# Kernel optimization log

Measured on AMD Instinct MI355X. Metric: run time of the kernel, lower is better.

The kernel has to match this reference:

```python
import jax, jax.numpy as jnp
import numpy as np
import math

L, R, B, S, D = 103, 512, 2, 512, 768


def setup_inputs() -> dict:
    key = jax.random.key(0)
    ks = jax.random.split(key, 16)
    n = lambda k, sh, s=1.0: jax.random.normal(k, sh, jnp.float32) * s
    W = 0.02  # weight init scale keeps softmax logits well-conditioned
    return {
        "output": n(ks[0], (B, S, D)),              # BERT sequence output (backbone treated as feature extractor)
        "attention_mask": jnp.ones((B, S), jnp.int32),
        "laws": n(ks[1], (L, R, D)),                # precomputed law representations (laws_rep.pkl)
        "Wq": n(ks[2], (D, D), W), "bq": jnp.zeros((D,), jnp.float32),
        "Wk": n(ks[3], (D, D), W), "bk": jnp.zeros((D,), jnp.float32),
        "Wv": n(ks[4], (D, D), W), "bv": jnp.zeros((D,), jnp.float32),
        "w_law_d": n(ks[5], (D,), W), "b_law_d": jnp.zeros((1,), jnp.float32),
        "w_law1": n(ks[6], (R,), W), "b_law1": jnp.zeros((1,), jnp.float32),
        "w_accu_d": n(ks[7], (D,), W), "b_accu_d": jnp.zeros((1,), jnp.float32),
        "w_accu1": n(ks[8], (R,), W), "b_accu1": jnp.zeros((1,), jnp.float32),
        "W_accu2": n(ks[9], (119, L), W), "b_accu2": jnp.zeros((119,), jnp.float32),
        "w_term_d": n(ks[10], (D,), W), "b_term_d": jnp.zeros((1,), jnp.float32),
        "w_term1": n(ks[11], (R,), W), "b_term1": jnp.zeros((1,), jnp.float32),
        "W_term2": n(ks[12], (11, L), W), "b_term2": jnp.zeros((11,), jnp.float32),
    }


def _forward(output, mask_f, laws, Wq, bq, Wk, bk, Wv, bv,
             w_law_d, b_law_d, w_law1, b_law1,
             w_accu_d, b_accu_d, w_accu1, b_accu1, W_accu2, b_accu2,
             w_term_d, b_term_d, w_term1, b_term1, W_term2, b_term2):
    laws_q = laws @ Wq + bq          # [L,R,D]
    facts_k = output @ Wk + bk       # [B,S,D]
    facts_v = output @ Wv + bv       # [B,S,D]
    # relevance: [L,B,R,S]
    scores = jnp.einsum('lrd,bsd->lbrs', laws_q, facts_k) / math.sqrt(768)
    scores = scores + (1.0 - mask_f)[None, :, None, :] * -10000.0
    probs = jax.nn.softmax(scores, axis=-1)          # (dropout omitted: eval mode)
    a_facts = jnp.einsum('lbrs,bsd->lbrd', probs, facts_v)
    g = jnp.transpose(a_facts, (1, 0, 2, 3))         # [B,L,R,D]
    act = jnp.tanh
    # law head: law1(tanh(law_d(g)))  -> [B,L]
    law = act(jnp.einsum('blrd,d->blr', g, w_law_d) + b_law_d)
    law = jnp.einsum('blr,r->bl', law, w_law1) + b_law1
    # accu head: accu2(tanh(accu1(tanh(accu_d(g))))) -> [B,119]
    accu = act(jnp.einsum('blrd,d->blr', g, w_accu_d) + b_accu_d)
    accu = act(jnp.einsum('blr,r->bl', accu, w_accu1) + b_accu1)
    accu = accu @ W_accu2.T + b_accu2
    # term head -> [B,11]
    term = act(jnp.einsum('blrd,d->blr', g, w_term_d) + b_term_d)
    term = act(jnp.einsum('blr,r->bl', term, w_term1) + b_term1)
    term = term @ W_term2.T + b_term2
    return law, accu, term


def reference(output, attention_mask, laws, Wq, bq, Wk, bk, Wv, bv,
              w_law_d, b_law_d, w_law1, b_law1,
              w_accu_d, b_accu_d, w_accu1, b_accu1, W_accu2, b_accu2,
              w_term_d, b_term_d, w_term1, b_term1, W_term2, b_term2):
    mask_f = attention_mask.astype(jnp.float32)
    return _forward(output, mask_f, laws, Wq, bq, Wk, bk, Wv, bv,
                    w_law_d, b_law_d, w_law1, b_law1,
                    w_accu_d, b_accu_d, w_accu1, b_accu1, W_accu2, b_accu2,
                    w_term_d, b_term_d, w_term1, b_term1, W_term2, b_term2)
```

## Files before the change

### kernel.cpp

```cpp
#include <hip/hip_runtime.h>

static constexpr int nL = 103, nR = 512, nB = 2, nS = 512, nD = 768;
static constexpr float INV_SQRT_D = 0.03608439182435161f;

typedef short bf16x8 __attribute__((ext_vector_type(8)));
typedef float f32x4 __attribute__((ext_vector_type(4)));
typedef unsigned short u16;
typedef unsigned short ushort4v __attribute__((ext_vector_type(4)));
typedef unsigned short ushort8v __attribute__((ext_vector_type(8)));

static constexpr size_t OFF_OUTB = 0;
static constexpr size_t OFF_MBF  = 393216;
static constexpr size_t OFF_KQB  = 688128;
static constexpr size_t OFF_QBK  = 1081344;
static constexpr size_t OFF_WKBQ = OFF_QBK + 768;
static constexpr size_t OFF_WV3  = OFF_WKBQ + 768;
static constexpr size_t OFF_CST  = OFF_WV3 + 2304;
static constexpr size_t OFF_C    = OFF_CST + 4;
static constexpr size_t OFF_HV   = OFF_C + 1024;
static constexpr size_t OFF_SUM  = OFF_HV + 3072;

__device__ inline float wredsum(float v) {
#pragma unroll
  for (int o = 32; o; o >>= 1) v += __shfl_xor(v, o);
  return v;
}

__device__ inline u16 f2bf(float f) {
  unsigned u = __builtin_bit_cast(unsigned, f);
  u += 0x7FFFu + ((u >> 16) & 1u);
  return (u16)(u >> 16);
}

__device__ inline bf16x8 cvt8(float4 a, float4 b) {
  ushort8v u;
  u[0]=f2bf(a.x); u[1]=f2bf(a.y); u[2]=f2bf(a.z); u[3]=f2bf(a.w);
  u[4]=f2bf(b.x); u[5]=f2bf(b.y); u[6]=f2bf(b.z); u[7]=f2bf(b.w);
  return __builtin_bit_cast(bf16x8, u);
}

__global__ __launch_bounds__(256) void k_prep(
    const float* __restrict__ Wq, const float* __restrict__ Wk,
    const float* __restrict__ Wv, const float* __restrict__ bq,
    const float* __restrict__ bk, const float* __restrict__ bv,
    const float* __restrict__ wld, const float* __restrict__ wad,
    const float* __restrict__ wtd, const float* __restrict__ outp,
    float* __restrict__ ws) {
  int tid = threadIdx.x, lane = tid & 63, w = tid >> 6;
  int bid = blockIdx.x;
  if (bid < 192) {
    int row = bid * 4 + w;
    const float* wqr = Wq + (size_t)row * nD;
    const float* wkr = Wk + (size_t)row * nD;
    const float* wvr = Wv + (size_t)row * nD;
    float dq = 0.f, dk = 0.f, d0 = 0.f, d1 = 0.f, d2 = 0.f;
#pragma unroll
    for (int k = 0; k < 3; ++k) {
      int off = lane * 4 + k * 256;
      float4 q4 = *(const float4*)(wqr + off);
      float4 k4 = *(const float4*)(wkr + off);
      float4 v4 = *(const float4*)(wvr + off);
      float4 bk4 = *(const float4*)(bk + off);
      float4 bq4 = *(const float4*)(bq + off);
      float4 l4 = *(const float4*)(wld + off);
      float4 a4 = *(const float4*)(wad + off);
      float4 t4 = *(const float4*)(wtd + off);
      dq += q4.x*bk4.x + q4.y*bk4.y + q4.z*bk4.z + q4.w*bk4.w;
      dk += k4.x*bq4.x + k4.y*bq4.y + k4.z*bq4.z + k4.w*bq4.w;
      d0 += v4.x*l4.x + v4.y*l4.y + v4.z*l4.z + v4.w*l4.w;
      d1 += v4.x*a4.x + v4.y*a4.y + v4.z*a4.z + v4.w*a4.w;
      d2 += v4.x*t4.x + v4.y*t4.y + v4.z*t4.z + v4.w*t4.w;
    }
    dq = wredsum(dq); dk = wredsum(dk);
    d0 = wredsum(d0); d1 = wredsum(d1); d2 = wredsum(d2);
    if (lane == 0) {
      ws[OFF_QBK + row] = dq;
      ws[OFF_WKBQ + row] = dk;
      ws[OFF_WV3 + row] = d0;
      ws[OFF_WV3 + 768 + row] = d1;
      ws[OFF_WV3 + 1536 + row] = d2;
    }
  } else if (bid == 192) {
    if (tid < 64) {
      float c0 = 0.f, c1 = 0.f, c2 = 0.f, c3 = 0.f;
      for (int j = lane; j < nD; j += 64) {
        c0 += bq[j]*bk[j]; c1 += bv[j]*wld[j]; c2 += bv[j]*wad[j]; c3 += bv[j]*wtd[j];
      }
      c0 = wredsum(c0); c1 = wredsum(c1); c2 = wredsum(c2); c3 = wredsum(c3);
      if (lane == 0) {
        ws[OFF_CST+0] = c0; ws[OFF_CST+1] = c1; ws[OFF_CST+2] = c2; ws[OFF_CST+3] = c3;
      }
    }
    for (int i = tid; i < 3 * nB * nL; i += 256) ws[OFF_SUM + i] = 0.f;
  } else {
    u16* outb = (u16*)(ws + OFF_OUTB);
    size_t e = ((size_t)(bid - 193) * 256 + tid) * 16;
    float4 f0 = *(const float4*)(outp + e);
    float4 f1 = *(const float4*)(outp + e + 4);
    float4 f2 = *(const float4*)(outp + e + 8);
    float4 f3 = *(const float4*)(outp + e + 12);
    *(ushort8v*)(outb + e)     = __builtin_bit_cast(ushort8v, cvt8(f0, f1));
    *(ushort8v*)(outb + e + 8) = __builtin_bit_cast(ushort8v, cvt8(f2, f3));
  }
}

__global__ __launch_bounds__(256) void k_mmM_chv(
    const float* __restrict__ Wq, const float* __restrict__ Wk,
    const float* __restrict__ outp, float* __restrict__ ws) {
  int tid = threadIdx.x, lane = tid & 63, w = tid >> 6;
  int bid = blockIdx.x;
  if (bid < 144) {
    u16* Mbf = (u16*)(ws + OFF_MBF);
    const int ti = bid / 12, tj = bid % 12;
    const int c4 = lane & 15, q4 = lane >> 4, wr = w >> 1, wc = w & 1;
    f32x4 acc[2][2];
#pragma unroll
    for (int i = 0; i < 2; ++i)
#pragma unroll
      for (int j = 0; j < 2; ++j) acc[i][j] = (f32x4){0.f,0.f,0.f,0.f};
    const float* Ab[2]; const float* Bb[2];
#pragma unroll
    for (int i = 0; i < 2; ++i)
      Ab[i] = Wq + (size_t)(ti*64 + wr*32 + i*16 + c4) * nD + q4*8;
#pragma unroll
    for (int j = 0; j < 2; ++j)
      Bb[j] = Wk + (size_t)(tj*64 + wc*32 + j*16 + c4) * nD + q4*8;
    for (int kt = 0; kt < 24; ++kt) {
      bf16x8 af[2], bf[2];
#pragma unroll
      for (int i = 0; i < 2; ++i)
        af[i] = cvt8(*(const float4*)(Ab[i] + kt*32), *(const float4*)(Ab[i] + kt*32 + 4));
#pragma unroll
      for (int j = 0; j < 2; ++j)
        bf[j] = cvt8(*(const float4*)(Bb[j] + kt*32), *(const float4*)(Bb[j] + kt*32 + 4));
#pragma unroll
      for (int i = 0; i < 2; ++i)
#pragma unroll
        for (int j = 0; j < 2; ++j)
          acc[i][j] = __builtin_amdgcn_mfma_f32_16x16x32_bf16(af[i], bf[j], acc[i][j], 0, 0, 0);
    }
#pragma unroll
    for (int i = 0; i < 2; ++i)
#pragma unroll
      for (int j = 0; j < 2; ++j) {
        int n = tj*64 + wc*32 + j*16 + c4;
#pragma unroll
        for (int reg = 0; reg < 4; ++reg) {
          int m = ti*64 + wr*32 + i*16 + q4*4 + reg;
          Mbf[(size_t)m * nD + n] = f2bf(acc[i][j][reg]);
        }
      }
  } else {
    int idx = (bid - 144) * 4 + w;
    const float* row = outp + (size_t)idx * nD;
    const float* wkbq = ws + OFF_WKBQ;
    const float* wv0 = ws + OFF_WV3;
    const float* wv1 = ws + OFF_WV3 + 768;
    const float* wv2 = ws + OFF_WV3 + 1536;
    float a0 = 0.f, a1 = 0.f, a2 = 0.f, a3 = 0.f;
#pragma unroll
    for (int k = 0; k < 3; ++k) {
      int off = lane * 4 + k * 256;
      float4 o4 = *(const float4*)(row + off);
      float4 k4 = *(const float4*)(wkbq + off);
      float4 l4 = *(const float4*)(wv0 + off);
      float4 c4v = *(const float4*)(wv1 + off);
      float4 t4 = *(const float4*)(wv2 + off);
      a0 += o4.x*k4.x + o4.y*k4.y + o4.z*k4.z + o4.w*k4.w;
      a1 += o4.x*l4.x + o4.y*l4.y + o4.z*l4.z + o4.w*l4.w;
      a2 += o4.x*c4v.x + o4.y*c4v.y + o4.z*c4v.z + o4.w*c4v.w;
      a3 += o4.x*t4.x + o4.y*t4.y + o4.z*t4.z + o4.w*t4.w;
    }
    a0 = wredsum(a0); a1 = wredsum(a1); a2 = wredsum(a2); a3 = wredsum(a3);
    if (lane == 0) {
      ws[OFF_C + idx]         = a0 + ws[OFF_CST+0];
      ws[OFF_HV + idx]        = a1 + ws[OFF_CST+1];
      ws[OFF_HV + 1024 + idx] = a2 + ws[OFF_CST+2];
      ws[OFF_HV + 2048 + idx] = a3 + ws[OFF_CST+3];
    }
  }
}

__global__ __launch_bounds__(256) void k_mkq(float* __restrict__ ws) {
  const u16* outb = (const u16*)(ws + OFF_OUTB);
  const u16* Mbf  = (const u16*)(ws + OFF_MBF);
  u16* kqB = (u16*)(ws + OFF_KQB);
  const float* qbk = ws + OFF_QBK;
  int tid = threadIdx.x, lane = tid & 63, w = tid >> 6;
  const int c4 = lane & 15, q4 = lane >> 4, wr = w >> 1, wc = w & 1;
  const int ti = blockIdx.y, tj = blockIdx.x;
  f32x4 acc[2][2];
#pragma unroll
  for (int i = 0; i < 2; ++i)
#pragma unroll
    for (int j = 0; j < 2; ++j) acc[i][j] = (f32x4){0.f,0.f,0.f,0.f};
  const u16* Ab[2]; const u16* Bb[2];
#pragma unroll
  for (int i = 0; i < 2; ++i)
    Ab[i] = outb + (size_t)(ti*64 + wr*32 + i*16 + c4) * nD + q4*8;
#pragma unroll
  for (int j = 0; j < 2; ++j)
    Bb[j] = Mbf + (size_t)(tj*64 + wc*32 + j*16 + c4) * nD + q4*8;
  for (int kt = 0; kt < 24; ++kt) {
    bf16x8 af[2], bf[2];
#pragma unroll
    for (int i = 0; i < 2; ++i) af[i] = *(const bf16x8*)(Ab[i] + kt*32);
#pragma unroll
    for (int j = 0; j < 2; ++j) bf[j] = *(const bf16x8*)(Bb[j] + kt*32);
#pragma unroll
    for (int i = 0; i < 2; ++i)
#pragma unroll
      for (int j = 0; j < 2; ++j)
        acc[i][j] = __builtin_amdgcn_mfma_f32_16x16x32_bf16(af[i], bf[j], acc[i][j], 0, 0, 0);
  }
#pragma unroll
  for (int i = 0; i < 2; ++i)
#pragma unroll
    for (int j = 0; j < 2; ++j) {
      int n = tj*64 + wc*32 + j*16 + c4;
      float bb = qbk[n];
#pragma unroll
      for (int reg = 0; reg < 4; ++reg) {
        int m = ti*64 + wr*32 + i*16 + q4*4 + reg;
        kqB[(((size_t)(n >> 3)) << 13) + ((size_t)m << 3) + (n & 7)] =
            f2bf(acc[i][j][reg] + bb);
      }
    }
}

__global__ __launch_bounds__(512) void k_attn(
    const float* __restrict__ laws, const u16* __restrict__ kqB,
    const int* __restrict__ mask, float* __restrict__ ws,
    const float* __restrict__ bld, const float* __restrict__ wl1,
    const float* __restrict__ bad, const float* __restrict__ wa1,
    const float* __restrict__ btd, const float* __restrict__ wt1) {
  __shared__ u16 Abuf[2][64 * 40];
  __shared__ f32x4 redS[8][64];
  const int tid = threadIdx.x, lane = tid & 63, w = tid >> 6;
  const int c4 = lane & 15, q4 = lane >> 4;
  const int b = blockIdx.x, rt8 = blockIdx.y, l = blockIdx.z;

  const int sr = tid >> 3, sq = tid & 7;
  const float* Asrc = laws + ((size_t)l * nR + rt8 * 64 + sr) * nD + sq * 4;
  u16* Aw = &Abuf[0][sr * 40 + sq * 4];

  const u16* Bbase = kqB + ((size_t)q4 * 1024 + (size_t)b * nS + w * 64 + c4) * 8;

  float4 g0 = *(const float4*)(Asrc);
  bf16x8 Bc[4];
#pragma unroll
  for (int ct = 0; ct < 4; ++ct) Bc[ct] = *(const bf16x8*)(Bbase + ct * 128);
  float4 g1 = *(const float4*)(Asrc + 32);
  {
    ushort4v u;
    u[0]=f2bf(g0.x); u[1]=f2bf(g0.y); u[2]=f2bf(g0.z); u[3]=f2bf(g0.w);
    *(ushort4v*)Aw = u;
  }
  f32x4 acc[4][4];
#pragma unroll
  for (int rt = 0; rt < 4; ++rt)
#pragma unroll
    for (int ct = 0; ct < 4; ++ct) acc[rt][ct] = (f32x4){0.f,0.f,0.f,0.f};
  __syncthreads();

#pragma unroll
  for (int kt = 0; kt < 24; ++kt) {
    bf16x8 Bn[4];
    float4 g2;
    if (kt < 23) {
#pragma unroll
      for (int ct = 0; ct < 4; ++ct)
        Bn[ct] = *(const bf16x8*)(Bbase + (size_t)(kt + 1) * 32768 + ct * 128);
    }
    if (kt < 22)
      g2 = *(const float4*)(Asrc + (size_t)(kt + 2) * 32);
    const u16* Ab = &Abuf[kt & 1][0];
    bf16x8 af[4];
#pragma unroll
    for (int rt = 0; rt < 4; ++rt)
      af[rt] = *(const bf16x8*)&Ab[(rt * 16 + c4) * 40 + q4 * 8];
#pragma unroll
    for (int rt = 0; rt < 4; ++rt)
#pragma unroll
      for (int ct = 0; ct < 4; ++ct)
        acc[rt][ct] = __builtin_amdgcn_mfma_f32_16x16x32_bf16(af[rt], Bc[ct],
                                                              acc[rt][ct], 0, 0, 0);
    if (kt < 23) {
      ushort4v u;
      u[0]=f2bf(g1.x); u[1]=f2bf(g1.y); u[2]=f2bf(g1.z); u[3]=f2bf(g1.w);
      *(ushort4v*)(Aw + ((kt + 1) & 1) * (64 * 40)) = u;
      g1 = g2;
#pragma unroll
      for (int ct = 0; ct < 4; ++ct) Bc[ct] = Bn[ct];
    }
    __syncthreads();
  }

  const float* cp  = ws + OFF_C + (size_t)b * nS;
  const float* hlp = ws + OFF_HV + (size_t)b * nS;
  const float* hap = ws + OFF_HV + 1024 + (size_t)b * nS;
  const float* htp = ws + OFF_HV + 2048 + (size_t)b * nS;
  float cc[4], hl[4], ha[4], ht[4], ma[4];
#pragma unroll
  for (int ct = 0; ct < 4; ++ct) {
    int s = w * 64 + ct * 16 + c4;
    cc[ct] = cp[s]; hl[ct] = hlp[s]; ha[ct] = hap[s]; ht[ct] = htp[s];
    ma[ct] = (1.0f - (float)mask[b * nS + s]) * -10000.0f;
  }

#pragma unroll
  for (int rt = 0; rt < 4; ++rt) {
#pragma unroll
    for (int reg = 0; reg < 4; ++reg) {
      float sse = 0.f, spl = 0.f, spa = 0.f, spt = 0.f;
#pragma unroll
      for (int ct = 0; ct < 4; ++ct) {
        float x = (acc[rt][ct][reg] + cc[ct]) * INV_SQRT_D + ma[ct];
        float e = __expf(x);
        sse += e; spl += e * hl[ct]; spa += e * ha[ct]; spt += e * ht[ct];
      }
#pragma unroll
      for (int o = 1; o < 16; o <<= 1) {
        sse += __shfl_xor(sse, o);
        spl += __shfl_xor(spl, o);
        spa += __shfl_xor(spa, o);
        spt += __shfl_xor(spt, o);
      }
      if (c4 == 0)
        redS[w][rt * 16 + q4 * 4 + reg] = (f32x4){sse, spl, spa, spt};
    }
  }
  __syncthreads();

  if (w == 0) {
    int row = lane;
    f32x4 t = (f32x4){0.f,0.f,0.f,0.f};
#pragma unroll
    for (int wc = 0; wc < 8; ++wc) t += redS[wc][row];
    float inv = 1.0f / t[0];
    int r = rt8 * 64 + row;
    float cl = tanhf(t[1] * inv + bld[0]) * wl1[r];
    float ca = tanhf(t[2] * inv + bad[0]) * wa1[r];
    float ctv = tanhf(t[3] * inv + btd[0]) * wt1[r];
#pragma unroll
    for (int o = 1; o < 64; o <<= 1) {
      cl += __shfl_xor(cl, o);
      ca += __shfl_xor(ca, o);
      ctv += __shfl_xor(ctv, o);
    }
    if (lane == 0) {
      float* sums = ws + OFF_SUM;
      atomicAdd(&sums[b * nL + l], cl);
      atomicAdd(&sums[nB * nL + b * nL + l], ca);
      atomicAdd(&sums[2 * nB * nL + b * nL + l], ctv);
    }
  }
}

__global__ void k_final(const float* __restrict__ ws, float* __restrict__ out,
                        const float* __restrict__ bl1, const float* __restrict__ ba1,
                        const float* __restrict__ Wa2, const float* __restrict__ ba2,
                        const float* __restrict__ bt1, const float* __restrict__ Wt2,
                        const float* __restrict__ bt2) {
  __shared__ float abl[nB * nL], tbl[nB * nL];
  int t = threadIdx.x;
  const float* sl = ws + OFF_SUM;
  const float* sa = sl + nB * nL;
  const float* st = sa + nB * nL;
  if (t < nB * nL) {
    out[t] = sl[t] + bl1[0];
    abl[t] = tanhf(sa[t] + ba1[0]);
    tbl[t] = tanhf(st[t] + bt1[0]);
  }
  __syncthreads();
  for (int idx = t; idx < nB * 119; idx += 256) {
    int b = idx / 119, j = idx % 119;
    float a = ba2[j];
    for (int ll = 0; ll < nL; ++ll) a += Wa2[j * nL + ll] * abl[b * nL + ll];
    out[nB * nL + idx] = a;
  }
  for (int idx = t; idx < nB * 11; idx += 256) {
    int b = idx / 11, j = idx % 11;
    float a = bt2[j];
    for (int ll = 0; ll < nL; ++ll) a += Wt2[j * nL + ll] * tbl[b * nL + ll];
    out[nB * nL + nB * 119 + idx] = a;
  }
}

extern "C" void kernel_launch(void* const* d_in, const int* in_sizes, int n_in,
                              void* d_out, int out_size, void* d_ws, size_t ws_size,
                              hipStream_t stream) {
  (void)in_sizes; (void)n_in; (void)out_size; (void)ws_size;
  const float* outp = (const float*)d_in[0];
  const int*   mask = (const int*)d_in[1];
  const float* laws = (const float*)d_in[2];
  const float* Wq = (const float*)d_in[3];  const float* bq = (const float*)d_in[4];
  const float* Wk = (const float*)d_in[5];  const float* bk = (const float*)d_in[6];
  const float* Wv = (const float*)d_in[7];  const float* bv = (const float*)d_in[8];
  const float* wld = (const float*)d_in[9];  const float* bld = (const float*)d_in[10];
  const float* wl1 = (const float*)d_in[11]; const float* bl1 = (const float*)d_in[12];
  const float* wad = (const float*)d_in[13]; const float* bad = (const float*)d_in[14];
  const float* wa1 = (const float*)d_in[15]; const float* ba1 = (const float*)d_in[16];
  const float* Wa2 = (const float*)d_in[17]; const float* ba2 = (const float*)d_in[18];
  const float* wtd = (const float*)d_in[19]; const float* btd = (const float*)d_in[20];
  const float* wt1 = (const float*)d_in[21]; const float* bt1 = (const float*)d_in[22];
  const float* Wt2 = (const float*)d_in[23]; const float* bt2 = (const float*)d_in[24];
  float* ws = (float*)d_ws;
  float* fout = (float*)d_out;
  u16* kqB = (u16*)(ws + OFF_KQB);

  k_prep<<<385, 256, 0, stream>>>(Wq, Wk, Wv, bq, bk, bv, wld, wad, wtd, outp, ws);
  k_mmM_chv<<<400, 256, 0, stream>>>(Wq, Wk, outp, ws);
  k_mkq<<<dim3(12, 16), 256, 0, stream>>>(ws);
  k_attn<<<dim3(nB, 8, nL), 512, 0, stream>>>(laws, kqB, mask, ws,
                                              bld, wl1, bad, wa1, btd, wt1);
  k_final<<<1, 256, 0, stream>>>(ws, fout, bl1, ba1, Wa2, ba2, bt1, Wt2, bt2);
}
```

Before: 460.2 us.

## Stage A tiles in 192-wide K chunks to cut barriers in attention GEMM

```diff
diff --git a/kernel.cpp b/kernel.cpp
--- a/kernel.cpp
+++ b/kernel.cpp
@@ -234,7 +234,7 @@
     const float* __restrict__ bld, const float* __restrict__ wl1,
     const float* __restrict__ bad, const float* __restrict__ wa1,
     const float* __restrict__ btd, const float* __restrict__ wt1) {
-  __shared__ u16 Abuf[2][64 * 40];
+  __shared__ u16 Abuf[64 * 200];
   __shared__ f32x4 redS[8][64];
   const int tid = threadIdx.x, lane = tid & 63, w = tid >> 6;
   const int c4 = lane & 15, q4 = lane >> 4;
@@ -242,58 +242,62 @@
 
   const int sr = tid >> 3, sq = tid & 7;
   const float* Asrc = laws + ((size_t)l * nR + rt8 * 64 + sr) * nD + sq * 4;
-  u16* Aw = &Abuf[0][sr * 40 + sq * 4];
+  u16* Aw = &Abuf[sr * 200 + sq * 4];
 
   const u16* Bbase = kqB + ((size_t)q4 * 1024 + (size_t)b * nS + w * 64 + c4) * 8;
 
-  float4 g0 = *(const float4*)(Asrc);
-  bf16x8 Bc[4];
-#pragma unroll
-  for (int ct = 0; ct < 4; ++ct) Bc[ct] = *(const bf16x8*)(Bbase + ct * 128);
-  float4 g1 = *(const float4*)(Asrc + 32);
-  {
+  f32x4 acc[4][4];
+#pragma unroll
+  for (int rt = 0; rt < 4; ++rt)
+#pragma unroll
+    for (int ct = 0; ct < 4; ++ct) acc[rt][ct] = (f32x4){0.f,0.f,0.f,0.f};
+
+  float4 g[6];
+#pragma unroll
+  for (int i = 0; i < 6; ++i) g[i] = *(const float4*)(Asrc + i * 32);
+#pragma unroll
+  for (int i = 0; i < 6; ++i) {
     ushort4v u;
-    u[0]=f2bf(g0.x); u[1]=f2bf(g0.y); u[2]=f2bf(g0.z); u[3]=f2bf(g0.w);
-    *(ushort4v*)Aw = u;
-  }
-  f32x4 acc[4][4];
-#pragma unroll
-  for (int rt = 0; rt < 4; ++rt)
-#pragma unroll
-    for (int ct = 0; ct < 4; ++ct) acc[rt][ct] = (f32x4){0.f,0.f,0.f,0.f};
+    u[0]=f2bf(g[i].x); u[1]=f2bf(g[i].y); u[2]=f2bf(g[i].z); u[3]=f2bf(g[i].w);
+    *(ushort4v*)(Aw + i * 32) = u;
+  }
   __syncthreads();
 
 #pragma unroll
-  for (int kt = 0; kt < 24; ++kt) {
-    bf16x8 Bn[4];
-    float4 g2;
-    if (kt < 23) {
+  for (int s = 0; s < 4; ++s) {
+    if (s < 3) {
+#pragma unroll
+      for (int i = 0; i < 6; ++i)
+        g[i] = *(const float4*)(Asrc + (s + 1) * 192 + i * 32);
+    }
+#pragma unroll
+    for (int k6 = 0; k6 < 6; ++k6) {
+      const int kt = s * 6 + k6;
+      bf16x8 bf[4];
 #pragma unroll
       for (int ct = 0; ct < 4; ++ct)
-        Bn[ct] = *(const bf16x8*)(Bbase + (size_t)(kt + 1) * 32768 + ct * 128);
-    }
-    if (kt < 22)
-      g2 = *(const float4*)(Asrc + (size_t)(kt + 2) * 32);
-    const u16* Ab = &Abuf[kt & 1][0];
-    bf16x8 af[4];
-#pragma unroll
-    for (int rt = 0; rt < 4; ++rt)
-      af[rt] = *(const bf16x8*)&Ab[(rt * 16 + c4) * 40 + q4 * 8];
-#pragma unroll
-    for (int rt = 0; rt < 4; ++rt)
-#pragma unroll
-      for (int ct = 0; ct < 4; ++ct)
-        acc[rt][ct] = __builtin_amdgcn_mfma_f32_16x16x32_bf16(af[rt], Bc[ct],
-                                                              acc[rt][ct], 0, 0, 0);
-    if (kt < 23) {
-      ushort4v u;
-      u[0]=f2bf(g1.x); u[1]=f2bf(g1.y); u[2]=f2bf(g1.z); u[3]=f2bf(g1.w);
-      *(ushort4v*)(Aw + ((kt + 1) & 1) * (64 * 40)) = u;
-      g1 = g2;
-#pragma unroll
-      for (int ct = 0; ct < 4; ++ct) Bc[ct] = Bn[ct];
+        bf[ct] = *(const bf16x8*)(Bbase + (size_t)kt * 32768 + ct * 128);
+      bf16x8 af[4];
+#pragma unroll
+      for (int rt = 0; rt < 4; ++rt)
+        af[rt] = *(const bf16x8*)&Abuf[(rt * 16 + c4) * 200 + k6 * 32 + q4 * 8];
+#pragma unroll
+      for (int rt = 0; rt < 4; ++rt)
+#pragma unroll
+        for (int ct = 0; ct < 4; ++ct)
+          acc[rt][ct] = __builtin_amdgcn_mfma_f32_16x16x32_bf16(af[rt], bf[ct],
+                                                                acc[rt][ct], 0, 0, 0);
     }
     __syncthreads();
+    if (s < 3) {
+#pragma unroll
+      for (int i = 0; i < 6; ++i) {
+        ushort4v u;
+        u[0]=f2bf(g[i].x); u[1]=f2bf(g[i].y); u[2]=f2bf(g[i].z); u[3]=f2bf(g[i].w);
+        *(ushort4v*)(Aw + i * 32) = u;
+      }
+      __syncthreads();
+    }
   }
 
   const float* cp  = ws + OFF_C + (size_t)b * nS;
```

New measurement: 459.9 us. Within noise of the previous version (-0.1%).
